# Kernel tuning notes

Measured on AMD Instinct MI355X. Metric: run time of the kernel, lower is better.

## Reference

```python
import jax, jax.numpy as jnp
import numpy as np

B, C, P, D = 16, 16, 512, 256

def setup_inputs() -> dict:
    key = jax.random.key(0)
    ks = jax.random.split(key, 5)
    return {
        "query": jax.random.normal(ks[0], (B, C, P, D), dtype=jnp.float32),
        "attn_weight": jax.random.normal(ks[1], (C, P, D), dtype=jnp.float32) * (1.0 / np.sqrt(D)),
        "q_proj_weight": jax.random.normal(ks[2], (C, D, D), dtype=jnp.float32) * (1.0 / np.sqrt(D)),
        "k_proj_weight": jax.random.normal(ks[3], (C, D, D), dtype=jnp.float32) * (1.0 / np.sqrt(D)),
        "v_proj_weight": jax.random.normal(ks[4], (C, D, D), dtype=jnp.float32) * (1.0 / np.sqrt(D)),
        "q_proj_bias": jnp.zeros((C, 1, D), dtype=jnp.float32),
        "k_proj_bias": jnp.zeros((C, 1, D), dtype=jnp.float32),
        "v_proj_bias": jnp.zeros((C, 1, D), dtype=jnp.float32),
    }

def reference(query, attn_weight, q_proj_weight, k_proj_weight, v_proj_weight,
              q_proj_bias, k_proj_bias, v_proj_bias):
    d = query.shape[-1]
    # cross-cycle context: sum over cycles minus own contribution
    acw = attn_weight * query                      # (B,C,P,D)
    context = acw.sum(axis=-3, keepdims=True) - acw  # (B,C,P,D)
    # per-cycle batched projections with ReLU
    q = jax.nn.relu(jnp.einsum('bcpd,cde->bcpe', query, q_proj_weight) + q_proj_bias)
    k = jax.nn.relu(jnp.einsum('bcpd,cde->bcpe', context, k_proj_weight) + k_proj_bias)
    v = jax.nn.relu(jnp.einsum('bcpd,cde->bcpe', context, v_proj_weight) + v_proj_bias)
    q = q * (float(d) ** -0.5)
    scores = jnp.einsum('bcpe,bcqe->bcpq', q, k)   # (B,C,P,P)
    attn = jax.nn.softmax(scores, axis=-1)         # dropout p=0.0 -> identity
    out = jnp.einsum('bcpq,bcqe->bcpe', attn, v)   # (B,C,P,D)
    return out
```

## Files before the change

### kernel.cpp

```cpp
#include <hip/hip_runtime.h>
#include <math.h>

#define B_ 16
#define C_ 16
#define P_ 512
#define D_ 256

constexpr int HEADS = B_ * C_;
constexpr int PD    = P_ * D_;
constexpr float QSCALE = 0.0625f;

typedef __attribute__((ext_vector_type(8))) short short8;
typedef __attribute__((ext_vector_type(4))) short short4_t;
typedef __attribute__((ext_vector_type(4))) float floatx4;

#define MFMA_BF16 __builtin_amdgcn_mfma_f32_16x16x32_bf16

__device__ inline short2 split_hl(float x) {
    unsigned xb = __float_as_uint(x);
    unsigned hb = (xb + 0x8000u) & 0xFFFF0000u;
    float lf = x - __uint_as_float(hb);
    short2 r;
    r.x = (short)(hb >> 16);
    r.y = (short)((__float_as_uint(lf) + 0x8000u) >> 16);
    return r;
}
__device__ inline unsigned packsplit(float x) {
    short2 s = split_hl(x);
    return (unsigned)(unsigned short)s.x | ((unsigned)(unsigned short)s.y << 16);
}

__device__ inline void gload16(const unsigned* g, unsigned* l) {
    __builtin_amdgcn_global_load_lds(
        (__attribute__((address_space(1))) void*)(g),
        (__attribute__((address_space(3))) void*)(l), 16, 0, 0);
}

__device__ inline void stage_sw(const unsigned* __restrict__ g, int gstride,
                                unsigned* lds, int tid) {
    int wv = tid >> 6, lane = tid & 63;
    int rsub = lane >> 3, slot = lane & 7;
#pragma unroll
    for (int it = 0; it < 4; ++it) {
        int r0 = it * 32 + wv * 8;
        int row = r0 + rsub;
        const unsigned* src = g + (size_t)row * gstride + ((slot ^ (row & 7)) << 2);
        gload16(src, &lds[r0 * 32]);
    }
}

__device__ inline void unpack8(const uint4& a, const uint4& b, short8& h, short8& l) {
    union { unsigned u[4]; short8 s; } H, L;
    H.u[0] = __builtin_amdgcn_perm(a.y, a.x, 0x05040100u);
    L.u[0] = __builtin_amdgcn_perm(a.y, a.x, 0x07060302u);
    H.u[1] = __builtin_amdgcn_perm(a.w, a.z, 0x05040100u);
    L.u[1] = __builtin_amdgcn_perm(a.w, a.z, 0x07060302u);
    H.u[2] = __builtin_amdgcn_perm(b.y, b.x, 0x05040100u);
    L.u[2] = __builtin_amdgcn_perm(b.y, b.x, 0x07060302u);
    H.u[3] = __builtin_amdgcn_perm(b.w, b.z, 0x05040100u);
    L.u[3] = __builtin_amdgcn_perm(b.w, b.z, 0x07060302u);
    h = H.s; l = L.s;
}

__device__ inline void rdfrag_sw(const unsigned* lds, int r, int hi,
                                 short8& h, short8& l) {
    int base = r * 32;
    int x = r & 7;
    const uint4 a = *reinterpret_cast<const uint4*>(&lds[base + ((((hi << 1))     ^ x) << 2)]);
    const uint4 b = *reinterpret_cast<const uint4*>(&lds[base + ((((hi << 1) | 1) ^ x) << 2)]);
    unpack8(a, b, h, l);
}

__device__ inline void rdfrag_pad(const unsigned* lds, int r, int hi,
                                  short8& h, short8& l) {
    const uint4 a = *reinterpret_cast<const uint4*>(&lds[r * 36 + hi * 8]);
    const uint4 b = *reinterpret_cast<const uint4*>(&lds[r * 36 + hi * 8 + 4]);
    unpack8(a, b, h, l);
}

__global__ __launch_bounds__(256) void k_sum_acw(const float* __restrict__ query,
                                                 const float* __restrict__ aw,
                                                 float* __restrict__ S) {
    int idx = blockIdx.x * 256 + threadIdx.x;
    int e = idx * 4;
    int d = e % D_;
    int p = (e / D_) % P_;
    int b = e / (D_ * P_);
    const float4* q4 = reinterpret_cast<const float4*>(query);
    const float4* a4 = reinterpret_cast<const float4*>(aw);
    int qbase = (((b * C_) * P_ + p) * D_ + d) >> 2;
    int abase = (p * D_ + d) >> 2;
    float4 acc = {0.f, 0.f, 0.f, 0.f};
#pragma unroll
    for (int c = 0; c < C_; ++c) {
        float4 qv = q4[qbase + c * (PD / 4)];
        float4 av = a4[abase + c * (PD / 4)];
        acc.x += qv.x * av.x;
        acc.y += qv.y * av.y;
        acc.z += qv.z * av.z;
        acc.w += qv.w * av.w;
    }
    reinterpret_cast<float4*>(S)[idx] = acc;
}

__global__ __launch_bounds__(256) void k_wpack(const float* __restrict__ Wq,
                                               const float* __restrict__ Wk,
                                               const float* __restrict__ Wv,
                                               unsigned* __restrict__ W2t) {
    __shared__ float tile[64][68];
    int wsel = blockIdx.z / C_;
    int c    = blockIdx.z % C_;
    int k0 = blockIdx.x * 64, n0 = blockIdx.y * 64;
    const float* Wsrc = wsel == 0 ? Wq : (wsel == 1 ? Wk : Wv);
    int tid = threadIdx.x;
#pragma unroll
    for (int it = 0; it < 4; ++it) {
        int idx = tid + it * 256;
        int kr = idx >> 4, nc = (idx & 15) * 4;
        float4 f = *reinterpret_cast<const float4*>(
            &Wsrc[(size_t)(c * D_ + k0 + kr) * D_ + n0 + nc]);
        *reinterpret_cast<float4*>(&tile[kr][nc]) = f;
    }
    __syncthreads();
#pragma unroll
    for (int it = 0; it < 4; ++it) {
        int idx = tid + it * 256;
        int nr = idx >> 4, kc = (idx & 15) * 4;
        uint4 u;
        u.x = packsplit(tile[kc + 0][nr]);
        u.y = packsplit(tile[kc + 1][nr]);
        u.z = packsplit(tile[kc + 2][nr]);
        u.w = packsplit(tile[kc + 3][nr]);
        *reinterpret_cast<uint4*>(
            &W2t[((size_t)(wsel * C_ + c) * D_ + n0 + nr) * D_ + k0 + kc]) = u;
    }
}

__global__ __launch_bounds__(256) void k_proj_mfma(
    const float* __restrict__ query, const float* __restrict__ aw,
    const float* __restrict__ S, const unsigned* __restrict__ W2t,
    const float* __restrict__ bq, const float* __restrict__ bk,
    const float* __restrict__ bv,
    unsigned* __restrict__ Q2, unsigned* __restrict__ K2,
    unsigned* __restrict__ V2t, int head0) {
    __shared__ unsigned Aw[2][128 * 36];
    __shared__ unsigned Bw[2][128 * 32];
    int tid = threadIdx.x;
    int lane = tid & 63, wv = tid >> 6;
    int wm = wv >> 1, wn = wv & 1;
    int ln = lane & 15, hi = lane >> 4, quad4 = hi * 4;
    int n0 = blockIdx.x * 128;
    int m0 = blockIdx.y * 128;
    int lh = blockIdx.z / 3, oid = blockIdx.z % 3;
    int hd = head0 + lh;
    int b = hd / C_, c = hd % C_;
    const unsigned* Wt = W2t + (size_t)(oid * C_ + c) * D_ * D_;

    int arow = tid >> 3, ack = (tid & 7) * 4;

    floatx4 acc[4][4] = {};

    stage_sw(Wt + (size_t)n0 * D_, D_, &Bw[0][0], tid);
#pragma unroll
    for (int it = 0; it < 4; ++it) {
        int row = arow + it * 32;
        float4 qv = *reinterpret_cast<const float4*>(
            &query[(size_t)(hd * P_ + m0 + row) * D_ + ack]);
        float x0, x1, x2, x3;
        if (oid == 0) {
            x0 = qv.x; x1 = qv.y; x2 = qv.z; x3 = qv.w;
        } else {
            float4 sv = *reinterpret_cast<const float4*>(
                &S[(size_t)(b * P_ + m0 + row) * D_ + ack]);
            float4 av = *reinterpret_cast<const float4*>(
                &aw[(size_t)(c * P_ + m0 + row) * D_ + ack]);
            x0 = sv.x - av.x * qv.x; x1 = sv.y - av.y * qv.y;
            x2 = sv.z - av.z * qv.z; x3 = sv.w - av.w * qv.w;
        }
        uint4 u;
        u.x = packsplit(x0); u.y = packsplit(x1);
        u.z = packsplit(x2); u.w = packsplit(x3);
        *reinterpret_cast<uint4*>(&Aw[0][row * 36 + ack]) = u;
    }
    __syncthreads();

    int cur = 0;
    for (int t = 0; t < 8; ++t) {
        int nx = cur ^ 1;
        bool pf = t < 7;
        int kk = (t + 1) * 32;
        if (pf) stage_sw(Wt + (size_t)n0 * D_ + kk, D_, &Bw[nx][0], tid);
        float4 qv[4], sv[4], av[4];
        if (pf) {
#pragma unroll
            for (int it = 0; it < 4; ++it) {
                int row = arow + it * 32;
                qv[it] = *reinterpret_cast<const float4*>(
                    &query[(size_t)(hd * P_ + m0 + row) * D_ + kk + ack]);
                if (oid != 0) {
                    sv[it] = *reinterpret_cast<const float4*>(
                        &S[(size_t)(b * P_ + m0 + row) * D_ + kk + ack]);
                    av[it] = *reinterpret_cast<const float4*>(
                        &aw[(size_t)(c * P_ + m0 + row) * D_ + kk + ack]);
                }
            }
        }
        short8 ah[4], alo[4], bh[4], blo[4];
#pragma unroll
        for (int i = 0; i < 4; ++i) {
            rdfrag_pad(&Aw[cur][0], wm * 64 + i * 16 + ln, hi, ah[i], alo[i]);
            rdfrag_sw(&Bw[cur][0], wn * 64 + i * 16 + ln, hi, bh[i], blo[i]);
        }
#pragma unroll
        for (int i = 0; i < 4; ++i)
#pragma unroll
            for (int j = 0; j < 4; ++j) {
                acc[i][j] = MFMA_BF16(ah[i], bh[j], acc[i][j], 0, 0, 0);
                acc[i][j] = MFMA_BF16(ah[i], blo[j], acc[i][j], 0, 0, 0);
                acc[i][j] = MFMA_BF16(alo[i], bh[j], acc[i][j], 0, 0, 0);
            }
        if (pf) {
#pragma unroll
            for (int it = 0; it < 4; ++it) {
                int row = arow + it * 32;
                float x0, x1, x2, x3;
                if (oid == 0) {
                    x0 = qv[it].x; x1 = qv[it].y; x2 = qv[it].z; x3 = qv[it].w;
                } else {
                    x0 = sv[it].x - av[it].x * qv[it].x;
                    x1 = sv[it].y - av[it].y * qv[it].y;
                    x2 = sv[it].z - av[it].z * qv[it].z;
                    x3 = sv[it].w - av[it].w * qv[it].w;
                }
                uint4 u;
                u.x = packsplit(x0); u.y = packsplit(x1);
                u.z = packsplit(x2); u.w = packsplit(x3);
                *reinterpret_cast<uint4*>(&Aw[nx][row * 36 + ack]) = u;
            }
        }
        __syncthreads();
        cur = nx;
    }

    const float* bias = oid == 0 ? bq : (oid == 1 ? bk : bv);
    float scale = oid == 0 ? QSCALE : 1.0f;
#pragma unroll
    for (int j = 0; j < 4; ++j) {
        int n_g = n0 + wn * 64 + j * 16 + ln;
        float bb = bias[c * D_ + n_g];
#pragma unroll
        for (int i = 0; i < 4; ++i) {
            int p0 = m0 + wm * 64 + i * 16 + quad4;
            if (oid == 2) {
                uint4 u;
                u.x = packsplit(fmaxf(acc[i][j][0] + bb, 0.f));
                u.y = packsplit(fmaxf(acc[i][j][1] + bb, 0.f));
                u.z = packsplit(fmaxf(acc[i][j][2] + bb, 0.f));
                u.w = packsplit(fmaxf(acc[i][j][3] + bb, 0.f));
                *reinterpret_cast<uint4*>(&V2t[(size_t)(lh * D_ + n_g) * P_ + p0]) = u;
            } else {
                unsigned* dst = oid == 0 ? Q2 : K2;
#pragma unroll
                for (int r = 0; r < 4; ++r) {
                    float v = fmaxf(acc[i][j][r] + bb, 0.f) * scale;
                    dst[(size_t)(lh * P_ + p0 + r) * D_ + n_g] = packsplit(v);
                }
            }
        }
    }
}

__global__ __launch_bounds__(256) void k_scores_mfma(
    const unsigned* __restrict__ Q2, const unsigned* __restrict__ K2,
    float* __restrict__ Sc) {
    __shared__ unsigned Aw[2][128 * 32];
    __shared__ unsigned Bw[2][128 * 32];
    int tid = threadIdx.x;
    int lane = tid & 63, wv = tid >> 6;
    int wm = wv >> 1, wn = wv & 1;
    int ln = lane & 15, hi = lane >> 4, quad4 = hi * 4;
    int n0 = blockIdx.x * 128;
    int m0 = blockIdx.y * 128;
    int lh = blockIdx.z;
    const unsigned* ga = Q2 + ((size_t)lh * P_ + m0) * D_;
    const unsigned* gb = K2 + ((size_t)lh * P_ + n0) * D_;

    floatx4 acc[4][4] = {};

    stage_sw(ga, D_, &Aw[0][0], tid);
    stage_sw(gb, D_, &Bw[0][0], tid);
    __syncthreads();

    int cur = 0;
    for (int t = 0; t < 8; ++t) {
        int nx = cur ^ 1;
        bool pf = t < 7;
        int kk = (t + 1) * 32;
        if (pf) {
            stage_sw(ga + kk, D_, &Aw[nx][0], tid);
            stage_sw(gb + kk, D_, &Bw[nx][0], tid);
        }
        short8 ah[4], alo[4], bh[4], blo[4];
#pragma unroll
        for (int i = 0; i < 4; ++i) {
            rdfrag_sw(&Aw[cur][0], wm * 64 + i * 16 + ln, hi, ah[i], alo[i]);
            rdfrag_sw(&Bw[cur][0], wn * 64 + i * 16 + ln, hi, bh[i], blo[i]);
        }
#pragma unroll
        for (int i = 0; i < 4; ++i)
#pragma unroll
            for (int j = 0; j < 4; ++j) {
                acc[i][j] = MFMA_BF16(ah[i], bh[j], acc[i][j], 0, 0, 0);
                acc[i][j] = MFMA_BF16(ah[i], blo[j], acc[i][j], 0, 0, 0);
                acc[i][j] = MFMA_BF16(alo[i], bh[j], acc[i][j], 0, 0, 0);
            }
        __syncthreads();
        cur = nx;
    }
#pragma unroll
    for (int j = 0; j < 4; ++j) {
        int n_g = n0 + wn * 64 + j * 16 + ln;
#pragma unroll
        for (int i = 0; i < 4; ++i) {
            int p0 = m0 + wm * 64 + i * 16 + quad4;
#pragma unroll
            for (int r = 0; r < 4; ++r)
                Sc[(size_t)lh * P_ * P_ + (size_t)(p0 + r) * P_ + n_g] = acc[i][j][r];
        }
    }
}

__global__ __launch_bounds__(256) void k_softmax_pack(float* __restrict__ Sc) {
    __shared__ float red[4];
    size_t row = blockIdx.x;
    int tid = threadIdx.x;
    float* r = Sc + row * P_;
    float v0 = r[tid], v1 = r[tid + 256];
    int lane = tid & 63, wid = tid >> 6;

    float m = fmaxf(v0, v1);
#pragma unroll
    for (int off = 32; off; off >>= 1) m = fmaxf(m, __shfl_xor(m, off));
    if (lane == 0) red[wid] = m;
    __syncthreads();
    m = fmaxf(fmaxf(red[0], red[1]), fmaxf(red[2], red[3]));
    __syncthreads();

    float e0 = __expf(v0 - m), e1 = __expf(v1 - m);
    float s = e0 + e1;
#pragma unroll
    for (int off = 32; off; off >>= 1) s += __shfl_xor(s, off);
    if (lane == 0) red[wid] = s;
    __syncthreads();
    s = red[0] + red[1] + red[2] + red[3];
    float inv = 1.0f / s;
    unsigned* w = reinterpret_cast<unsigned*>(r);
    w[tid] = packsplit(e0 * inv);
    w[tid + 256] = packsplit(e1 * inv);
}

__global__ __launch_bounds__(256) void k_out_mfma(
    const unsigned* __restrict__ A2, const unsigned* __restrict__ V2t,
    float* __restrict__ O, int head0) {
    __shared__ unsigned Aw[2][128 * 32];
    __shared__ unsigned Bw[2][128 * 32];
    int tid = threadIdx.x;
    int lane = tid & 63, wv = tid >> 6;
    int wm = wv >> 1, wn = wv & 1;
    int ln = lane & 15, hi = lane >> 4, quad4 = hi * 4;
    int n0 = blockIdx.x * 128;
    int m0 = blockIdx.y * 128;
    int lh = blockIdx.z;
    int hd = head0 + lh;
    const unsigned* ga = A2 + (size_t)lh * P_ * P_ + (size_t)m0 * P_;
    const unsigned* gb = V2t + ((size_t)lh * D_ + n0) * P_;

    floatx4 acc[4][4] = {};

    stage_sw(ga, P_, &Aw[0][0], tid);
    stage_sw(gb, P_, &Bw[0][0], tid);
    __syncthreads();

    int cur = 0;
    for (int t = 0; t < 16; ++t) {
        int nx = cur ^ 1;
        bool pf = t < 15;
        int kk = (t + 1) * 32;
        if (pf) {
            stage_sw(ga + kk, P_, &Aw[nx][0], tid);
            stage_sw(gb + kk, P_, &Bw[nx][0], tid);
        }
        short8 ah[4], alo[4], bh[4], blo[4];
#pragma unroll
        for (int i = 0; i < 4; ++i) {
            rdfrag_sw(&Aw[cur][0], wm * 64 + i * 16 + ln, hi, ah[i], alo[i]);
            rdfrag_sw(&Bw[cur][0], wn * 64 + i * 16 + ln, hi, bh[i], blo[i]);
        }
#pragma unroll
        for (int i = 0; i < 4; ++i)
#pragma unroll
            for (int j = 0; j < 4; ++j) {
                acc[i][j] = MFMA_BF16(ah[i], bh[j], acc[i][j], 0, 0, 0);
                acc[i][j] = MFMA_BF16(ah[i], blo[j], acc[i][j], 0, 0, 0);
                acc[i][j] = MFMA_BF16(alo[i], bh[j], acc[i][j], 0, 0, 0);
            }
        __syncthreads();
        cur = nx;
    }
#pragma unroll
    for (int j = 0; j < 4; ++j) {
        int n_g = n0 + wn * 64 + j * 16 + ln;
#pragma unroll
        for (int i = 0; i < 4; ++i) {
            int p0 = m0 + wm * 64 + i * 16 + quad4;
#pragma unroll
            for (int r = 0; r < 4; ++r)
                O[(size_t)(hd * P_ + p0 + r) * D_ + n_g] = acc[i][j][r];
        }
    }
}

extern "C" void kernel_launch(void* const* d_in, const int* in_sizes, int n_in,
                              void* d_out, int out_size, void* d_ws, size_t ws_size,
                              hipStream_t stream) {
    (void)in_sizes; (void)n_in; (void)out_size;
    const float* query = (const float*)d_in[0];
    const float* aw    = (const float*)d_in[1];
    const float* Wq    = (const float*)d_in[2];
    const float* Wk    = (const float*)d_in[3];
    const float* Wv    = (const float*)d_in[4];
    const float* bq    = (const float*)d_in[5];
    const float* bk    = (const float*)d_in[6];
    const float* bv    = (const float*)d_in[7];
    float* out = (float*)d_out;

    char* ws = (char*)d_ws;
    const size_t s_words   = (size_t)B_ * P_ * D_;
    const size_t w2t_words = (size_t)3 * C_ * D_ * D_;
    const size_t fixed_bytes = (s_words + w2t_words) * 4;
    const size_t per_head_bytes = ((size_t)3 * P_ * D_ + (size_t)P_ * P_) * 4;
    size_t avail = ws_size > fixed_bytes ? ws_size - fixed_bytes : 0;
    int H = (int)(avail / per_head_bytes);
    if (H < 1) H = 1;
    if (H > HEADS) H = HEADS;

    float*    S   = (float*)ws;
    unsigned* W2t = (unsigned*)(ws + s_words * 4);
    unsigned* Q2  = (unsigned*)(ws + fixed_bytes);
    unsigned* K2  = Q2 + (size_t)H * P_ * D_;
    unsigned* V2t = K2 + (size_t)H * P_ * D_;
    float*    Sc  = (float*)(V2t + (size_t)H * P_ * D_);

    k_sum_acw<<<(B_ * P_ * D_ / 4) / 256, 256, 0, stream>>>(query, aw, S);
    k_wpack<<<dim3(D_ / 64, D_ / 64, 3 * C_), 256, 0, stream>>>(Wq, Wk, Wv, W2t);

    for (int head0 = 0; head0 < HEADS; head0 += H) {
        int Hc = HEADS - head0 < H ? HEADS - head0 : H;
        k_proj_mfma<<<dim3(D_ / 128, P_ / 128, 3 * Hc), 256, 0, stream>>>(
            query, aw, S, W2t, bq, bk, bv, Q2, K2, V2t, head0);
        k_scores_mfma<<<dim3(P_ / 128, P_ / 128, Hc), 256, 0, stream>>>(Q2, K2, Sc);
        k_softmax_pack<<<Hc * P_, 256, 0, stream>>>(Sc);
        k_out_mfma<<<dim3(D_ / 128, P_ / 128, Hc), 256, 0, stream>>>(
            (const unsigned*)Sc, V2t, out, head0);
    }
}
```

Baseline: 1.074 ms.

## Fuse scores, softmax and PV into a single flash-attention kernel

Replaces the separate scores GEMM, softmax-pack and output GEMM kernels with one fused kernel that uses online softmax over 128-wide key blocks. Each 512-thread block owns 128 query rows of one head. Q/K and V chunks are streamed through shared memory, and the probabilities are staged per wave in LDS as split bf16. This removes the P×P score matrix round trip through global memory and two launches per head chunk, and frees workspace so more heads fit per chunk. In exchange it uses more registers (16 output accumulators per wave) and more shared memory. Q chunks are also re-staged for every key block.

```diff
diff --git a/kernel.cpp b/kernel.cpp
--- a/kernel.cpp
+++ b/kernel.cpp
@@ -43,6 +43,19 @@
 #pragma unroll
     for (int it = 0; it < 4; ++it) {
         int r0 = it * 32 + wv * 8;
+        int row = r0 + rsub;
+        const unsigned* src = g + (size_t)row * gstride + ((slot ^ (row & 7)) << 2);
+        gload16(src, &lds[r0 * 32]);
+    }
+}
+
+__device__ inline void stage_sw8(const unsigned* __restrict__ g, int gstride,
+                                 unsigned* lds, int tid) {
+    int wv = tid >> 6, lane = tid & 63;
+    int rsub = lane >> 3, slot = lane & 7;
+#pragma unroll
+    for (int it = 0; it < 2; ++it) {
+        int r0 = it * 64 + wv * 8;
         int row = r0 + rsub;
         const unsigned* src = g + (size_t)row * gstride + ((slot ^ (row & 7)) << 2);
         gload16(src, &lds[r0 * 32]);
@@ -270,152 +283,142 @@
     }
 }
 
-__global__ __launch_bounds__(256) void k_scores_mfma(
+__global__ __launch_bounds__(512) void k_attn(
     const unsigned* __restrict__ Q2, const unsigned* __restrict__ K2,
-    float* __restrict__ Sc) {
-    __shared__ unsigned Aw[2][128 * 32];
-    __shared__ unsigned Bw[2][128 * 32];
+    const unsigned* __restrict__ V2t, float* __restrict__ O, int head0) {
+    __shared__ unsigned chunk[4][128 * 32];
+    __shared__ unsigned Pl[8][16 * 128];
     int tid = threadIdx.x;
     int lane = tid & 63, wv = tid >> 6;
-    int wm = wv >> 1, wn = wv & 1;
-    int ln = lane & 15, hi = lane >> 4, quad4 = hi * 4;
-    int n0 = blockIdx.x * 128;
+    int ln = lane & 15, hi = lane >> 4;
+    int lh = blockIdx.x;
     int m0 = blockIdx.y * 128;
-    int lh = blockIdx.z;
-    const unsigned* ga = Q2 + ((size_t)lh * P_ + m0) * D_;
-    const unsigned* gb = K2 + ((size_t)lh * P_ + n0) * D_;
-
-    floatx4 acc[4][4] = {};
-
-    stage_sw(ga, D_, &Aw[0][0], tid);
-    stage_sw(gb, D_, &Bw[0][0], tid);
+    int hd = head0 + lh;
+    const unsigned* gq = Q2 + ((size_t)lh * P_ + m0) * D_;
+    const unsigned* gk = K2 + (size_t)lh * P_ * D_;
+    const unsigned* gv = V2t + (size_t)lh * D_ * P_;
+    unsigned* myP = &Pl[wv][0];
+
+    floatx4 o[16] = {};
+    float m_[4], l_[4];
+#pragma unroll
+    for (int r = 0; r < 4; ++r) { m_[r] = -INFINITY; l_[r] = 0.f; }
+
+    stage_sw8(gq, D_, chunk[0], tid);
+    stage_sw8(gk, D_, chunk[2], tid);
     __syncthreads();
-
     int cur = 0;
-    for (int t = 0; t < 8; ++t) {
-        int nx = cur ^ 1;
-        bool pf = t < 7;
-        int kk = (t + 1) * 32;
-        if (pf) {
-            stage_sw(ga + kk, D_, &Aw[nx][0], tid);
-            stage_sw(gb + kk, D_, &Bw[nx][0], tid);
-        }
-        short8 ah[4], alo[4], bh[4], blo[4];
-#pragma unroll
-        for (int i = 0; i < 4; ++i) {
-            rdfrag_sw(&Aw[cur][0], wm * 64 + i * 16 + ln, hi, ah[i], alo[i]);
-            rdfrag_sw(&Bw[cur][0], wn * 64 + i * 16 + ln, hi, bh[i], blo[i]);
-        }
-#pragma unroll
-        for (int i = 0; i < 4; ++i)
-#pragma unroll
-            for (int j = 0; j < 4; ++j) {
-                acc[i][j] = MFMA_BF16(ah[i], bh[j], acc[i][j], 0, 0, 0);
-                acc[i][j] = MFMA_BF16(ah[i], blo[j], acc[i][j], 0, 0, 0);
-                acc[i][j] = MFMA_BF16(alo[i], bh[j], acc[i][j], 0, 0, 0);
-            }
-        __syncthreads();
-        cur = nx;
-    }
-#pragma unroll
-    for (int j = 0; j < 4; ++j) {
-        int n_g = n0 + wn * 64 + j * 16 + ln;
-#pragma unroll
-        for (int i = 0; i < 4; ++i) {
-            int p0 = m0 + wm * 64 + i * 16 + quad4;
-#pragma unroll
-            for (int r = 0; r < 4; ++r)
-                Sc[(size_t)lh * P_ * P_ + (size_t)(p0 + r) * P_ + n_g] = acc[i][j][r];
-        }
-    }
-}
-
-__global__ __launch_bounds__(256) void k_softmax_pack(float* __restrict__ Sc) {
-    __shared__ float red[4];
-    size_t row = blockIdx.x;
-    int tid = threadIdx.x;
-    float* r = Sc + row * P_;
-    float v0 = r[tid], v1 = r[tid + 256];
-    int lane = tid & 63, wid = tid >> 6;
-
-    float m = fmaxf(v0, v1);
-#pragma unroll
-    for (int off = 32; off; off >>= 1) m = fmaxf(m, __shfl_xor(m, off));
-    if (lane == 0) red[wid] = m;
-    __syncthreads();
-    m = fmaxf(fmaxf(red[0], red[1]), fmaxf(red[2], red[3]));
-    __syncthreads();
-
-    float e0 = __expf(v0 - m), e1 = __expf(v1 - m);
-    float s = e0 + e1;
-#pragma unroll
-    for (int off = 32; off; off >>= 1) s += __shfl_xor(s, off);
-    if (lane == 0) red[wid] = s;
-    __syncthreads();
-    s = red[0] + red[1] + red[2] + red[3];
-    float inv = 1.0f / s;
-    unsigned* w = reinterpret_cast<unsigned*>(r);
-    w[tid] = packsplit(e0 * inv);
-    w[tid + 256] = packsplit(e1 * inv);
-}
-
-__global__ __launch_bounds__(256) void k_out_mfma(
-    const unsigned* __restrict__ A2, const unsigned* __restrict__ V2t,
-    float* __restrict__ O, int head0) {
-    __shared__ unsigned Aw[2][128 * 32];
-    __shared__ unsigned Bw[2][128 * 32];
-    int tid = threadIdx.x;
-    int lane = tid & 63, wv = tid >> 6;
-    int wm = wv >> 1, wn = wv & 1;
-    int ln = lane & 15, hi = lane >> 4, quad4 = hi * 4;
-    int n0 = blockIdx.x * 128;
-    int m0 = blockIdx.y * 128;
-    int lh = blockIdx.z;
-    int hd = head0 + lh;
-    const unsigned* ga = A2 + (size_t)lh * P_ * P_ + (size_t)m0 * P_;
-    const unsigned* gb = V2t + ((size_t)lh * D_ + n0) * P_;
-
-    floatx4 acc[4][4] = {};
-
-    stage_sw(ga, P_, &Aw[0][0], tid);
-    stage_sw(gb, P_, &Bw[0][0], tid);
-    __syncthreads();
-
-    int cur = 0;
-    for (int t = 0; t < 16; ++t) {
-        int nx = cur ^ 1;
-        bool pf = t < 15;
-        int kk = (t + 1) * 32;
-        if (pf) {
-            stage_sw(ga + kk, P_, &Aw[nx][0], tid);
-            stage_sw(gb + kk, P_, &Bw[nx][0], tid);
-        }
-        short8 ah[4], alo[4], bh[4], blo[4];
-#pragma unroll
-        for (int i = 0; i < 4; ++i) {
-            rdfrag_sw(&Aw[cur][0], wm * 64 + i * 16 + ln, hi, ah[i], alo[i]);
-            rdfrag_sw(&Bw[cur][0], wn * 64 + i * 16 + ln, hi, bh[i], blo[i]);
-        }
-#pragma unroll
-        for (int i = 0; i < 4; ++i)
-#pragma unroll
-            for (int j = 0; j < 4; ++j) {
-                acc[i][j] = MFMA_BF16(ah[i], bh[j], acc[i][j], 0, 0, 0);
-                acc[i][j] = MFMA_BF16(ah[i], blo[j], acc[i][j], 0, 0, 0);
-                acc[i][j] = MFMA_BF16(alo[i], bh[j], acc[i][j], 0, 0, 0);
-            }
-        __syncthreads();
-        cur = nx;
-    }
-#pragma unroll
-    for (int j = 0; j < 4; ++j) {
-        int n_g = n0 + wn * 64 + j * 16 + ln;
-#pragma unroll
-        for (int i = 0; i < 4; ++i) {
-            int p0 = m0 + wm * 64 + i * 16 + quad4;
-#pragma unroll
-            for (int r = 0; r < 4; ++r)
-                O[(size_t)(hd * P_ + p0 + r) * D_ + n_g] = acc[i][j][r];
+
+    for (int kv = 0; kv < 4; ++kv) {
+        floatx4 s_[8] = {};
+        for (int kk = 0; kk < 8; ++kk) {
+            int nx = cur ^ 1;
+            if (kk < 7) {
+                stage_sw8(gq + (kk + 1) * 32, D_, chunk[nx], tid);
+                stage_sw8(gk + (size_t)(kv * 128) * D_ + (kk + 1) * 32, D_,
+                          chunk[2 + nx], tid);
+            } else {
+                stage_sw8(gv + kv * 128, P_, chunk[nx], tid);
+                stage_sw8(gv + (size_t)128 * P_ + kv * 128, P_, chunk[2 + nx], tid);
+            }
+            short8 ah, al_, bh, bl_;
+            rdfrag_sw(chunk[cur], wv * 16 + ln, hi, ah, al_);
+            __builtin_amdgcn_s_setprio(1);
+#pragma unroll
+            for (int j = 0; j < 8; ++j) {
+                rdfrag_sw(chunk[2 + cur], j * 16 + ln, hi, bh, bl_);
+                s_[j] = MFMA_BF16(ah, bh, s_[j], 0, 0, 0);
+                s_[j] = MFMA_BF16(ah, bl_, s_[j], 0, 0, 0);
+                s_[j] = MFMA_BF16(al_, bh, s_[j], 0, 0, 0);
+            }
+            __builtin_amdgcn_s_setprio(0);
+            __syncthreads();
+            cur = nx;
+        }
+
+        float sc[4], rs[4];
+#pragma unroll
+        for (int r = 0; r < 4; ++r) {
+            float mx = s_[0][r];
+#pragma unroll
+            for (int j = 1; j < 8; ++j) mx = fmaxf(mx, s_[j][r]);
+            mx = fmaxf(mx, __shfl_xor(mx, 1));
+            mx = fmaxf(mx, __shfl_xor(mx, 2));
+            mx = fmaxf(mx, __shfl_xor(mx, 4));
+            mx = fmaxf(mx, __shfl_xor(mx, 8));
+            float mn = fmaxf(m_[r], mx);
+            sc[r] = __expf(m_[r] - mn);
+            m_[r] = mn;
+            rs[r] = 0.f;
+        }
+#pragma unroll
+        for (int n = 0; n < 16; ++n)
+#pragma unroll
+            for (int r = 0; r < 4; ++r) o[n][r] *= sc[r];
+
+#pragma unroll
+        for (int j = 0; j < 8; ++j)
+#pragma unroll
+            for (int r = 0; r < 4; ++r) {
+                float p = __expf(s_[j][r] - m_[r]);
+                rs[r] += p;
+                int row = hi * 4 + r, col = j * 16 + ln;
+                int slot = (col >> 2) ^ (row & 7);
+                myP[row * 128 + slot * 4 + (col & 3)] = packsplit(p);
+            }
+#pragma unroll
+        for (int r = 0; r < 4; ++r) {
+            float s = rs[r];
+            s += __shfl_xor(s, 1);
+            s += __shfl_xor(s, 2);
+            s += __shfl_xor(s, 4);
+            s += __shfl_xor(s, 8);
+            l_[r] = l_[r] * sc[r] + s;
+        }
+
+        for (int kq = 0; kq < 4; ++kq) {
+            int nx = cur ^ 1;
+            if (kq < 3) {
+                stage_sw8(gv + kv * 128 + (kq + 1) * 32, P_, chunk[nx], tid);
+                stage_sw8(gv + (size_t)128 * P_ + kv * 128 + (kq + 1) * 32, P_,
+                          chunk[2 + nx], tid);
+            } else if (kv < 3) {
+                stage_sw8(gq, D_, chunk[nx], tid);
+                stage_sw8(gk + (size_t)((kv + 1) * 128) * D_, D_, chunk[2 + nx], tid);
+            }
+            int x = ln & 7;
+            const uint4 a0 = *reinterpret_cast<const uint4*>(
+                &myP[ln * 128 + (((kq * 8 + 2 * hi)) ^ x) * 4]);
+            const uint4 a1 = *reinterpret_cast<const uint4*>(
+                &myP[ln * 128 + (((kq * 8 + 2 * hi + 1)) ^ x) * 4]);
+            short8 pah, pal;
+            unpack8(a0, a1, pah, pal);
+            __builtin_amdgcn_s_setprio(1);
+#pragma unroll
+            for (int n = 0; n < 16; ++n) {
+                short8 vh, vl;
+                const unsigned* vb = (n < 8) ? chunk[cur] : chunk[2 + cur];
+                rdfrag_sw(vb, (n & 7) * 16 + ln, hi, vh, vl);
+                o[n] = MFMA_BF16(pah, vh, o[n], 0, 0, 0);
+                o[n] = MFMA_BF16(pah, vl, o[n], 0, 0, 0);
+                o[n] = MFMA_BF16(pal, vh, o[n], 0, 0, 0);
+            }
+            __builtin_amdgcn_s_setprio(0);
+            __syncthreads();
+            cur = nx;
+        }
+    }
+
+    float inv[4];
+#pragma unroll
+    for (int r = 0; r < 4; ++r) inv[r] = 1.0f / l_[r];
+#pragma unroll
+    for (int n = 0; n < 16; ++n) {
+        int col = n * 16 + ln;
+#pragma unroll
+        for (int r = 0; r < 4; ++r) {
+            int row = m0 + wv * 16 + hi * 4 + r;
+            O[((size_t)hd * P_ + row) * D_ + col] = o[n][r] * inv[r];
         }
     }
 }
@@ -438,7 +441,7 @@
     const size_t s_words   = (size_t)B_ * P_ * D_;
     const size_t w2t_words = (size_t)3 * C_ * D_ * D_;
     const size_t fixed_bytes = (s_words + w2t_words) * 4;
-    const size_t per_head_bytes = ((size_t)3 * P_ * D_ + (size_t)P_ * P_) * 4;
+    const size_t per_head_bytes = (size_t)3 * P_ * D_ * 4;
     size_t avail = ws_size > fixed_bytes ? ws_size - fixed_bytes : 0;
     int H = (int)(avail / per_head_bytes);
     if (H < 1) H = 1;
@@ -449,7 +452,6 @@
     unsigned* Q2  = (unsigned*)(ws + fixed_bytes);
     unsigned* K2  = Q2 + (size_t)H * P_ * D_;
     unsigned* V2t = K2 + (size_t)H * P_ * D_;
-    float*    Sc  = (float*)(V2t + (size_t)H * P_ * D_);
 
     k_sum_acw<<<(B_ * P_ * D_ / 4) / 256, 256, 0, stream>>>(query, aw, S);
     k_wpack<<<dim3(D_ / 64, D_ / 64, 3 * C_), 256, 0, stream>>>(Wq, Wk, Wv, W2t);
@@ -458,9 +460,6 @@
         int Hc = HEADS - head0 < H ? HEADS - head0 : H;
         k_proj_mfma<<<dim3(D_ / 128, P_ / 128, 3 * Hc), 256, 0, stream>>>(
             query, aw, S, W2t, bq, bk, bv, Q2, K2, V2t, head0);
-        k_scores_mfma<<<dim3(P_ / 128, P_ / 128, Hc), 256, 0, stream>>>(Q2, K2, Sc);
-        k_softmax_pack<<<Hc * P_, 256, 0, stream>>>(Sc);
-        k_out_mfma<<<dim3(D_ / 128, P_ / 128, Hc), 256, 0, stream>>>(
-            (const unsigned*)Sc, V2t, out, head0);
-    }
-}
+        k_attn<<<dim3(Hc, P_ / 128), 512, 0, stream>>>(Q2, K2, V2t, out, head0);
+    }
+}
```

Result: faster. 919.1 us (-14.4%).
